# Performance work log

Hardware: AMD Instinct MI355X
Metric: run time of the kernel (lower is better)

The kernel has to match this reference:

```python
import jax, jax.numpy as jnp
import numpy as np

B, NS, NT, C = 32, 1000, 100, 256
LAMBDA_GIOU, LAMBDA_L1 = 10.0, 1.0


def _lsa(cost):
    """Hungarian / Jonker-Volgenant shortest-augmenting-path (numpy, O(n^2 m)).
    Matches scipy.optimize.linear_sum_assignment for rectangular matrices."""
    cost = np.asarray(cost, dtype=np.float64)
    transposed = cost.shape[0] > cost.shape[1]
    if transposed:
        cost = cost.T
    n, m = cost.shape  # n <= m
    INF = np.inf
    u = np.zeros(n + 1)
    v = np.zeros(m + 1)
    p = np.zeros(m + 1, dtype=np.int64)   # p[j] = row (1-based) assigned to col j
    way = np.zeros(m + 1, dtype=np.int64)
    for i in range(1, n + 1):
        p[0] = i
        j0 = 0
        minv = np.full(m + 1, INF)
        used = np.zeros(m + 1, dtype=bool)
        while True:
            used[j0] = True
            i0 = p[j0]
            cur = cost[i0 - 1, :] - u[i0] - v[1:]
            free = ~used[1:]
            better = free & (cur < minv[1:])
            minv[1:][better] = cur[better]
            way[1:][better] = j0
            masked = np.where(free, minv[1:], INF)
            j1 = int(np.argmin(masked)) + 1
            delta = masked[j1 - 1]
            u[p[used]] += delta
            v[used] -= delta
            minv[~used] -= delta
            j0 = j1
            if p[j0] == 0:
                break
        while j0:
            j1 = way[j0]
            p[j0] = p[j1]
            j0 = j1
    rows = p[1:] - 1
    cols = np.arange(m)
    keep = rows >= 0
    rows, cols = rows[keep], cols[keep]
    if transposed:
        rows, cols = cols, rows
    order = np.argsort(rows)
    return rows[order], cols[order]


def _pairwise_cost(logits, classes, sb, tb):
    """Per-batch (Ns,Nt) cost = CE(logits_s, class_t) + 10*(1-GIoU(box_s, box_t)) + L1mean."""
    Bc, Ns, Cd = logits.shape
    Nt = classes.shape[1]
    # Cross entropy: logsumexp over classes minus logit at target class (identical
    # math to the torch expand+flatten CE, without the Ns*Nt*C copy).
    lse = jax.nn.logsumexp(logits, axis=-1)  # (B,Ns)
    picked = jnp.take_along_axis(
        logits, jnp.broadcast_to(classes[:, None, :], (Bc, Ns, Nt)), axis=2)  # (B,Ns,Nt)
    ce = lse[:, :, None] - picked
    # Pairwise GIoU (boxes in xyxy)
    s = sb[:, :, None, :]  # (B,Ns,1,4)
    t = tb[:, None, :, :]  # (B,1,Nt,4)
    ix1 = jnp.maximum(s[..., 0], t[..., 0])
    iy1 = jnp.maximum(s[..., 1], t[..., 1])
    ix2 = jnp.minimum(s[..., 2], t[..., 2])
    iy2 = jnp.minimum(s[..., 3], t[..., 3])
    inter = jnp.clip(ix2 - ix1, 0.0) * jnp.clip(iy2 - iy1, 0.0)
    area_s = (s[..., 2] - s[..., 0]) * (s[..., 3] - s[..., 1])
    area_t = (t[..., 2] - t[..., 0]) * (t[..., 3] - t[..., 1])
    union = area_s + area_t - inter
    iou = inter / union
    cx1 = jnp.minimum(s[..., 0], t[..., 0])
    cy1 = jnp.minimum(s[..., 1], t[..., 1])
    cx2 = jnp.maximum(s[..., 2], t[..., 2])
    cy2 = jnp.maximum(s[..., 3], t[..., 3])
    carea = (cx2 - cx1) * (cy2 - cy1)
    giou = iou - (carea - union) / carea
    l1 = jnp.abs(s - t).mean(axis=-1)  # (B,Ns,Nt)
    return ce + LAMBDA_GIOU * (1.0 - giou) + LAMBDA_L1 * l1


def _valid_boxes(key, b, n):
    p = jax.random.uniform(key, (b, n, 2, 2), dtype=jnp.float32)
    lo = p.min(axis=2)
    hi = p.max(axis=2)
    return jnp.concatenate([lo, hi], axis=-1)  # (b,n,4) xyxy, x1<x2, y1<y2


def setup_inputs() -> dict:
    key = jax.random.key(0)
    k1, k2, k3, k4 = jax.random.split(key, 4)
    return {
        "source_class_logits": jax.random.normal(k1, (B, NS, C), dtype=jnp.float32),
        "target_classes": jax.random.randint(k2, (B, NT), 0, C, dtype=jnp.int32),
        "source_boxes": _valid_boxes(k3, B, NS),
        "target_boxes": _valid_boxes(k4, B, NT),
    }


def reference(source_class_logits, target_classes, source_boxes, target_boxes):
    cost = _pairwise_cost(source_class_logits, target_classes, source_boxes, target_boxes)
    cost_np = np.asarray(cost)
    rows_l, cols_l = [], []
    for b in range(cost_np.shape[0]):  # assignment is inherently per-matrix / host-side
        r, c = _lsa(cost_np[b])
        rows_l.append(r)
        cols_l.append(c)
    rows = jnp.asarray(np.stack(rows_l))  # (B, min(Ns,Nt))
    cols = jnp.asarray(np.stack(cols_l))
    bidx = jnp.arange(cost.shape[0])[:, None]
    return cost[bidx, rows, cols].mean(axis=1)  # (B,)
```

## Files before the change

### kernel.cpp

```cpp
#include <hip/hip_runtime.h>
#include <math.h>

#define NSRC 1000
#define NTGT 100
#define NCLS 256
#define NB   32
#define NSP  1024
#define PAD_IDX(j) ((j) + ((j) >> 4))
#define LDSN (NSP + (NSP >> 4))
#define AUCTION_EPS 0.01f
#define NWAVES 4
#define ROUND_CAP 128


__global__ __launch_bounds__(256) void lse_kernel(const float* __restrict__ logits,
                                                  float* __restrict__ lse) {
    int wid  = threadIdx.x >> 6;
    int lane = threadIdx.x & 63;
    int row0 = blockIdx.x * 32 + wid * 8;
    #pragma unroll 2
    for (int r = 0; r < 8; ++r) {
        int row = row0 + r;
        float4 v4 = reinterpret_cast<const float4*>(logits + (size_t)row * NCLS)[lane];
        float m = fmaxf(fmaxf(v4.x, v4.y), fmaxf(v4.z, v4.w));
        #pragma unroll
        for (int off = 32; off >= 1; off >>= 1) m = fmaxf(m, __shfl_xor(m, off));
        float s = expf(v4.x - m) + expf(v4.y - m) + expf(v4.z - m) + expf(v4.w - m);
        #pragma unroll
        for (int off = 32; off >= 1; off >>= 1) s += __shfl_xor(s, off);
        if (lane == 0) lse[row] = m + logf(s);
    }
}

__global__ __launch_bounds__(256) void cost_kernel(const float* __restrict__ logits,
                                                   const int*   __restrict__ tcls,
                                                   const float* __restrict__ sbox,
                                                   const float* __restrict__ tbox,
                                                   const float* __restrict__ lse,
                                                   float*       __restrict__ cost,
                                                   float*       __restrict__ urow_g,
                                                   int*         __restrict__ jmin_g,
                                                   float*       __restrict__ m2_g) {
    int b  = blockIdx.x & 31;
    int t  = blockIdx.x >> 5;
    int bt = b * NTGT + t;
    int cls = tcls[bt];
    float4 tb = reinterpret_cast<const float4*>(tbox)[bt];
    float area_t = (tb.z - tb.x) * (tb.w - tb.y);
    float* crow = cost + (size_t)bt * NSP;
    float m1 = 1e38f, m2 = 1e38f; int mi = 0x7fffffff;
    for (int s = threadIdx.x; s < NSP; s += 256) {
        if (s >= NSRC) { crow[s] = 1e30f; continue; }
        int gs = b * NSRC + s;
        float4 sb = reinterpret_cast<const float4*>(sbox)[gs];
        float ce = lse[gs] - logits[(size_t)gs * NCLS + cls];
        float ix1 = fmaxf(sb.x, tb.x), iy1 = fmaxf(sb.y, tb.y);
        float ix2 = fminf(sb.z, tb.z), iy2 = fminf(sb.w, tb.w);
        float inter = fmaxf(ix2 - ix1, 0.f) * fmaxf(iy2 - iy1, 0.f);
        float area_s = (sb.z - sb.x) * (sb.w - sb.y);
        float uni = area_s + area_t - inter;
        float iou = inter / uni;
        float cx1 = fminf(sb.x, tb.x), cy1 = fminf(sb.y, tb.y);
        float cx2 = fmaxf(sb.z, tb.z), cy2 = fmaxf(sb.w, tb.w);
        float carea = (cx2 - cx1) * (cy2 - cy1);
        float giou = iou - (carea - uni) / carea;
        float l1 = 0.25f * (fabsf(sb.x - tb.x) + fabsf(sb.y - tb.y) +
                            fabsf(sb.z - tb.z) + fabsf(sb.w - tb.w));
        float c = ce + 10.0f * (1.0f - giou) + l1;
        crow[s] = c;
        if (c < m1) { m2 = m1; m1 = c; mi = s; }
        else if (c < m2) m2 = c;
    }
    #pragma unroll
    for (int off = 32; off >= 1; off >>= 1) {
        float om1 = __shfl_xor(m1, off);
        float om2 = __shfl_xor(m2, off);
        int   oi  = __shfl_xor(mi, off);
        bool take = (om1 < m1) || (om1 == m1 && oi < mi);
        float lose = take ? m1 : om1;
        m1 = take ? om1 : m1;
        mi = take ? oi  : mi;
        m2 = fminf(fminf(m2, om2), lose);
    }
    __shared__ float smin[4], smin2[4];
    __shared__ int   sidx[4];
    int wid = threadIdx.x >> 6, lane = threadIdx.x & 63;
    if (lane == 0) { smin[wid] = m1; smin2[wid] = m2; sidx[wid] = mi; }
    __syncthreads();
    if (threadIdx.x == 0) {
        #pragma unroll
        for (int w = 1; w < 4; ++w) {
            float om1 = smin[w], om2 = smin2[w]; int oi = sidx[w];
            bool take = (om1 < m1) || (om1 == m1 && oi < mi);
            float lose = take ? m1 : om1;
            m1 = take ? om1 : m1;
            mi = take ? oi  : mi;
            m2 = fminf(fminf(m2, om2), lose);
        }
        urow_g[bt] = m1;
        jmin_g[bt] = mi;
        m2_g[bt]   = m2;
    }
}

__global__ __launch_bounds__(256) void lsa_kernel(const float* __restrict__ cost,
                                                  const float* __restrict__ urow_g,
                                                  const int*   __restrict__ jmin_g,
                                                  const float* __restrict__ m2_g,
                                                  float* __restrict__ out) {
    int b    = blockIdx.x;
    int tid  = threadIdx.x;
    int wv   = tid >> 6;
    int lane = tid & 63;
    const float* C = cost + (size_t)b * NTGT * NSP;
    __shared__ int   way[LDSN];
    __shared__ int   pcol[LDSN];
    __shared__ float uu[LDSN];
    __shared__ float vsh[LDSN];
    __shared__ float urow[NTGT];
    __shared__ float m2s[NTGT];
    __shared__ int   jmin[NTGT];
    __shared__ int   done[NTGT];
    __shared__ int   qbuf[1024];
    __shared__ int   qstate[2];
    __shared__ int   srow[NWAVES], scol[NWAVES];
    __shared__ float sm1[NWAVES], sm2[NWAVES], svscan[NWAVES];

    for (int t = tid; t < LDSN; t += 256) {
        pcol[t] = -1; uu[t] = 0.f; vsh[t] = 0.f; way[t] = 0x7fffffff;
    }
    for (int t = tid; t < NTGT; t += 256) {
        urow[t] = urow_g[b * NTGT + t];
        jmin[t] = jmin_g[b * NTGT + t];
        m2s[t]  = m2_g[b * NTGT + t];
    }
    if (tid == 0) { qstate[0] = 0; qstate[1] = 0; }
    __syncthreads();

    for (int r = tid; r < NTGT; r += 256) atomicMin(&way[PAD_IDX(jmin[r])], r);
    __syncthreads();
    for (int r = tid; r < NTGT; r += 256) {
        int j = jmin[r];
        int w = (way[PAD_IDX(j)] == r) ? 1 : 0;
        done[r] = w;
        if (w) { pcol[PAD_IDX(j)] = r; uu[PAD_IDX(j)] = urow[r]; }
    }
    __syncthreads();

    if (tid < 64) {
        int qt = 0;
        #pragma unroll
        for (int r0 = 0; r0 < 128; r0 += 64) {
            int r = r0 + lane;
            bool act = (r < NTGT) && !done[r];
            unsigned long long mask = __ballot(act);
            if (act) qbuf[qt + __popcll(mask & ((1ull << lane) - 1ull))] = r;
            qt += __popcll(mask);
        }
        if (lane == 0) qstate[1] = qt;
    }
    __syncthreads();

    int base = lane * 16;

    for (int round = 0; round < ROUND_CAP; ++round) {
        int qh = qstate[0], qt = qstate[1];
        int navail = qt - qh;
        if (navail <= 0) break;
        int take = navail < NWAVES ? navail : NWAVES;
        if (wv < take) {
            int i = qbuf[(qh + wv) & 1023];
            int j1; float m1, m2;
            int pj = jmin[i];
            if (vsh[PAD_IDX(pj)] == 0.0f) {
                j1 = pj; m1 = urow[i]; m2 = m2s[i];
            } else {
                const float4* row4 = reinterpret_cast<const float4*>(C + (size_t)i * NSP + base);
                m1 = 1e38f; m2 = 1e38f; j1 = 0x7fffffff;
                #pragma unroll
                for (int q = 0; q < 4; ++q) {
                    float4 c4 = row4[q];
                    float vals[4];
                    vals[0] = c4.x - vsh[PAD_IDX(base + 4*q + 0)];
                    vals[1] = c4.y - vsh[PAD_IDX(base + 4*q + 1)];
                    vals[2] = c4.z - vsh[PAD_IDX(base + 4*q + 2)];
                    vals[3] = c4.w - vsh[PAD_IDX(base + 4*q + 3)];
                    #pragma unroll
                    for (int e = 0; e < 4; ++e) {
                        float val = vals[e];
                        if (val < m1) { m2 = m1; m1 = val; j1 = base + 4*q + e; }
                        else m2 = fminf(m2, val);
                    }
                }
                #pragma unroll
                for (int off = 32; off >= 1; off >>= 1) {
                    float om1 = __shfl_xor(m1, off);
                    float om2 = __shfl_xor(m2, off);
                    int   oj1 = __shfl_xor(j1, off);
                    bool take2 = (om1 < m1) || (om1 == m1 && oj1 < j1);
                    float lose = take2 ? m1 : om1;
                    m1 = take2 ? om1 : m1;
                    j1 = take2 ? oj1 : j1;
                    m2 = fminf(fminf(m2, om2), lose);
                }
            }
            if (lane == 0) {
                srow[wv] = i; scol[wv] = j1; sm1[wv] = m1; sm2[wv] = m2;
                svscan[wv] = vsh[PAD_IDX(j1)];
            }
        }
        __syncthreads();
        if (tid == 0) {
            int qt2 = qstate[1];
            for (int s = 0; s < take; ++s) {
                int i = srow[s], j1 = scol[s];
                int pj1 = PAD_IDX(j1);
                if (vsh[pj1] == svscan[s]) {
                    float delta = fmaxf(sm2[s] - sm1[s], AUCTION_EPS);
                    int old = pcol[pj1];
                    vsh[pj1]  = svscan[s] - delta;
                    pcol[pj1] = i;
                    uu[pj1]   = sm1[s] + delta;
                    urow[i]   = sm1[s] + delta;
                    done[i]   = 1;
                    if (old >= 0) { qbuf[qt2 & 1023] = old; ++qt2; done[old] = 0; }
                } else {
                    qbuf[qt2 & 1023] = i; ++qt2;
                }
            }
            qstate[0] = qstate[0] + take;
            qstate[1] = qt2;
        }
        __syncthreads();
    }

    float v[16], d[16];
    if (tid < 64) {
        #pragma unroll
        for (int k = 0; k < 16; ++k) v[k] = vsh[PAD_IDX(base + k)];
    }
    __syncthreads();

    for (int i = 0; i < NTGT; ++i) {
        if (done[i]) continue;
        float ui = urow[i];
        float Df = 0.f;
        int jf = -1;
        if (tid < 64) {
            const float4* row4 = reinterpret_cast<const float4*>(C + (size_t)i * NSP + base);
            #pragma unroll
            for (int q = 0; q < 4; ++q) {
                float4 c4 = row4[q];
                d[4*q+0] = c4.x - ui - v[4*q+0];
                d[4*q+1] = c4.y - ui - v[4*q+1];
                d[4*q+2] = c4.z - ui - v[4*q+2];
                d[4*q+3] = c4.w - ui - v[4*q+3];
            }
            #pragma unroll
            for (int k = 0; k < 16; ++k) way[PAD_IDX(base + k)] = -1;
            unsigned int used = 0;

            for (int it = 0; it < NTGT + 3; ++it) {
                float lmin = 1e38f;
                #pragma unroll
                for (int k = 0; k < 16; ++k) {
                    float val = ((used >> k) & 1u) ? 1e38f : d[k];
                    lmin = fminf(lmin, val);
                }
                float wmin = lmin;
                #pragma unroll
                for (int off = 32; off >= 1; off >>= 1) wmin = fminf(wmin, __shfl_xor(wmin, off));
                unsigned long long msk = __ballot(lmin == wmin);
                int src = __ffsll(msk) - 1;
                int myk = -1;
                #pragma unroll
                for (int k = 15; k >= 0; --k)
                    if (!((used >> k) & 1u) && d[k] == wmin) myk = k;
                int j0 = __shfl(base + myk, src);
                if (j0 < 0) break;
                int pj0 = pcol[PAD_IDX(j0)];
                if (pj0 < 0) { Df = wmin; jf = j0; break; }
                if ((j0 >> 4) == lane) used |= 1u << (j0 & 15);
                float uref = uu[PAD_IDX(j0)];
                float sft  = wmin - uref;
                const float4* rr = reinterpret_cast<const float4*>(C + (size_t)pj0 * NSP + base);
                float cr[16];
                #pragma unroll
                for (int q = 0; q < 4; ++q) {
                    float4 c4 = rr[q];
                    cr[4*q+0] = c4.x; cr[4*q+1] = c4.y; cr[4*q+2] = c4.z; cr[4*q+3] = c4.w;
                }
                #pragma unroll
                for (int k = 0; k < 16; ++k) {
                    float cand = sft + cr[k] - v[k];
                    bool upd = (cand < d[k]) && !((used >> k) & 1u);
                    if (upd) { d[k] = cand; way[PAD_IDX(base + k)] = j0; }
                }
            }

            if (jf >= 0) {
                #pragma unroll
                for (int k = 0; k < 16; ++k) {
                    if ((used >> k) & 1u) {
                        float diff = Df - d[k];
                        v[k] -= diff;
                        uu[PAD_IDX(base + k)] += diff;
                    }
                }
            }
        }
        __syncthreads();
        if (tid == 0 && jf >= 0) {
            int j = jf;
            for (int g = 0; g < NSP; ++g) {
                int jp = way[PAD_IDX(j)];
                if (jp < 0) { pcol[PAD_IDX(j)] = i; uu[PAD_IDX(j)] = ui + Df; break; }
                pcol[PAD_IDX(j)] = pcol[PAD_IDX(jp)];
                uu[PAD_IDX(j)]   = uu[PAD_IDX(jp)];
                j = jp;
            }
            done[i] = 1;
        }
        __syncthreads();
    }

    if (tid < 64) {
        float acc = 0.f;
        #pragma unroll
        for (int k = 0; k < 16; ++k) {
            int j = base + k;
            if (j < NSRC) {
                int r = pcol[PAD_IDX(j)];
                if (r >= 0) acc += C[(size_t)r * NSP + j];
            }
        }
        #pragma unroll
        for (int off = 32; off >= 1; off >>= 1) acc += __shfl_xor(acc, off);
        if (lane == 0) out[b] = acc * (1.0f / NTGT);
    }
}

extern "C" void kernel_launch(void* const* d_in, const int* in_sizes, int n_in,
                              void* d_out, int out_size, void* d_ws, size_t ws_size,
                              hipStream_t stream) {
    const float* logits = (const float*)d_in[0];
    const int*   tcls   = (const int*)  d_in[1];
    const float* sbox   = (const float*)d_in[2];
    const float* tbox   = (const float*)d_in[3];
    float* out = (float*)d_out;

    float* lse    = (float*)d_ws;
    float* cost   = lse + 32768;
    float* urow_g = cost + (size_t)NB * NTGT * NSP;
    int*   jmin_g = (int*)(urow_g + NB * NTGT);
    float* m2_g   = (float*)(jmin_g + NB * NTGT);

    lse_kernel <<<1000,      256, 0, stream>>>(logits, lse);
    cost_kernel<<<NB * NTGT, 256, 0, stream>>>(logits, tcls, sbox, tbox, lse, cost,
                                               urow_g, jmin_g, m2_g);
    lsa_kernel <<<NB,        256, 0, stream>>>(cost, urow_g, jmin_g, m2_g, out);
}
```

Measured before the change: 128.6 us.

## Cache per-row auction bids and double bidding waves in assignment kernel

The auction-based assignment kernel now keeps each row's last best column, best value, second-best value and the column price seen at scan time in shared memory. A row rescans its cost row only when its cached best, adjusted for later price drops on that column, exceeds its cached second-best. The kernel also runs with 512 threads, so 8 waves bid per round instead of 4, and the round cap rises to 160. The aim is to cut redundant global row scans and the number of serial rounds. In exchange, a single thread resolves more bids per round, and code not shown may assume the old 256-thread block size.

```diff
diff --git a/kernel.cpp b/kernel.cpp
--- a/kernel.cpp
+++ b/kernel.cpp
@@ -9,8 +9,8 @@
 #define PAD_IDX(j) ((j) + ((j) >> 4))
 #define LDSN (NSP + (NSP >> 4))
 #define AUCTION_EPS 0.01f
-#define NWAVES 4
-#define ROUND_CAP 128
+#define NWAVES 8
+#define ROUND_CAP 160
 
 
 __global__ __launch_bounds__(256) void lse_kernel(const float* __restrict__ logits,
@@ -103,7 +103,7 @@
     }
 }
 
-__global__ __launch_bounds__(256) void lsa_kernel(const float* __restrict__ cost,
+__global__ __launch_bounds__(512) void lsa_kernel(const float* __restrict__ cost,
                                                   const float* __restrict__ urow_g,
                                                   const int*   __restrict__ jmin_g,
                                                   const float* __restrict__ m2_g,
@@ -118,29 +118,33 @@
     __shared__ float uu[LDSN];
     __shared__ float vsh[LDSN];
     __shared__ float urow[NTGT];
-    __shared__ float m2s[NTGT];
-    __shared__ int   jmin[NTGT];
     __shared__ int   done[NTGT];
+    __shared__ float bm1[NTGT];
+    __shared__ float bm2[NTGT];
+    __shared__ int   bj [NTGT];
+    __shared__ float bv [NTGT];
     __shared__ int   qbuf[1024];
     __shared__ int   qstate[2];
-    __shared__ int   srow[NWAVES], scol[NWAVES];
-    __shared__ float sm1[NWAVES], sm2[NWAVES], svscan[NWAVES];
-
-    for (int t = tid; t < LDSN; t += 256) {
+    __shared__ int   srow[NWAVES];
+
+    for (int t = tid; t < LDSN; t += 512) {
         pcol[t] = -1; uu[t] = 0.f; vsh[t] = 0.f; way[t] = 0x7fffffff;
     }
-    for (int t = tid; t < NTGT; t += 256) {
-        urow[t] = urow_g[b * NTGT + t];
-        jmin[t] = jmin_g[b * NTGT + t];
-        m2s[t]  = m2_g[b * NTGT + t];
+    for (int t = tid; t < NTGT; t += 512) {
+        float m1 = urow_g[b * NTGT + t];
+        urow[t] = m1;
+        bm1[t]  = m1;
+        bm2[t]  = m2_g[b * NTGT + t];
+        bj[t]   = jmin_g[b * NTGT + t];
+        bv[t]   = 0.f;
     }
     if (tid == 0) { qstate[0] = 0; qstate[1] = 0; }
     __syncthreads();
 
-    for (int r = tid; r < NTGT; r += 256) atomicMin(&way[PAD_IDX(jmin[r])], r);
-    __syncthreads();
-    for (int r = tid; r < NTGT; r += 256) {
-        int j = jmin[r];
+    for (int r = tid; r < NTGT; r += 512) atomicMin(&way[PAD_IDX(bj[r])], r);
+    __syncthreads();
+    for (int r = tid; r < NTGT; r += 512) {
+        int j = bj[r];
         int w = (way[PAD_IDX(j)] == r) ? 1 : 0;
         done[r] = w;
         if (w) { pcol[PAD_IDX(j)] = r; uu[PAD_IDX(j)] = urow[r]; }
@@ -170,13 +174,11 @@
         int take = navail < NWAVES ? navail : NWAVES;
         if (wv < take) {
             int i = qbuf[(qh + wv) & 1023];
-            int j1; float m1, m2;
-            int pj = jmin[i];
-            if (vsh[PAD_IDX(pj)] == 0.0f) {
-                j1 = pj; m1 = urow[i]; m2 = m2s[i];
-            } else {
+            if (lane == 0) srow[wv] = i;
+            float m1p = bm1[i] + (bv[i] - vsh[PAD_IDX(bj[i])]);
+            if (m1p > bm2[i]) {
                 const float4* row4 = reinterpret_cast<const float4*>(C + (size_t)i * NSP + base);
-                m1 = 1e38f; m2 = 1e38f; j1 = 0x7fffffff;
+                float m1 = 1e38f, m2 = 1e38f; int j1 = 0x7fffffff;
                 #pragma unroll
                 for (int q = 0; q < 4; ++q) {
                     float4 c4 = row4[q];
@@ -197,31 +199,34 @@
                     float om1 = __shfl_xor(m1, off);
                     float om2 = __shfl_xor(m2, off);
                     int   oj1 = __shfl_xor(j1, off);
-                    bool take2 = (om1 < m1) || (om1 == m1 && oj1 < j1);
-                    float lose = take2 ? m1 : om1;
-                    m1 = take2 ? om1 : m1;
-                    j1 = take2 ? oj1 : j1;
+                    bool tk = (om1 < m1) || (om1 == m1 && oj1 < j1);
+                    float lose = tk ? m1 : om1;
+                    m1 = tk ? om1 : m1;
+                    j1 = tk ? oj1 : j1;
                     m2 = fminf(fminf(m2, om2), lose);
                 }
-            }
-            if (lane == 0) {
-                srow[wv] = i; scol[wv] = j1; sm1[wv] = m1; sm2[wv] = m2;
-                svscan[wv] = vsh[PAD_IDX(j1)];
+                if (lane == 0) {
+                    bm1[i] = m1; bm2[i] = m2; bj[i] = j1;
+                    bv[i]  = vsh[PAD_IDX(j1)];
+                }
             }
         }
         __syncthreads();
         if (tid == 0) {
             int qt2 = qstate[1];
             for (int s = 0; s < take; ++s) {
-                int i = srow[s], j1 = scol[s];
+                int i  = srow[s];
+                int j1 = bj[i];
                 int pj1 = PAD_IDX(j1);
-                if (vsh[pj1] == svscan[s]) {
-                    float delta = fmaxf(sm2[s] - sm1[s], AUCTION_EPS);
+                float vnow = vsh[pj1];
+                float m1p  = bm1[i] + (bv[i] - vnow);
+                if (m1p <= bm2[i]) {
+                    float delta = fmaxf(bm2[i] - m1p, AUCTION_EPS);
                     int old = pcol[pj1];
-                    vsh[pj1]  = svscan[s] - delta;
+                    vsh[pj1]  = vnow - delta;
                     pcol[pj1] = i;
-                    uu[pj1]   = sm1[s] + delta;
-                    urow[i]   = sm1[s] + delta;
+                    uu[pj1]   = m1p + delta;
+                    urow[i]   = m1p + delta;
                     done[i]   = 1;
                     if (old >= 0) { qbuf[qt2 & 1023] = old; ++qt2; done[old] = 0; }
                 } else {
@@ -358,5 +363,5 @@
     lse_kernel <<<1000,      256, 0, stream>>>(logits, lse);
     cost_kernel<<<NB * NTGT, 256, 0, stream>>>(logits, tcls, sbox, tbox, lse, cost,
                                                urow_g, jmin_g, m2_g);
-    lsa_kernel <<<NB,        256, 0, stream>>>(cost, urow_g, jmin_g, m2_g, out);
+    lsa_kernel <<<NB,        512, 0, stream>>>(cost, urow_g, jmin_g, m2_g, out);
 }
```

Measured after the change: 127.8 us. Within noise of the previous version (-0.7%).
